# Performance work log

Hardware: AMD Instinct MI355X
Metric: run time of the kernel (lower is better)

## Reference

```python
import jax, jax.numpy as jnp
import numpy as np

N = 50000   # nodes
E = 800000  # edges (avg degree 16)
IN = 64     # in_dim
DS = 32     # in_dim // 2
HOUT = 64


def setup_inputs() -> dict:
    key = jax.random.key(0)
    ks = jax.random.split(key, 16)
    std = 0.1

    def w(k, shape):
        return std * jax.random.normal(k, shape, dtype=jnp.float32)

    z = lambda d: jnp.zeros((d,), dtype=jnp.float32)
    return {
        "x": jax.random.normal(ks[0], (N, IN), dtype=jnp.float32),
        "src": jax.random.randint(ks[1], (E,), 0, N),
        "dst": jax.random.randint(ks[2], (E,), 0, N),
        # encoders (enc_dim == in_dim branch: dim_split -> dim_split)
        "WencK": w(ks[3], (DS, DS)), "bencK": z(DS),
        "WencP1": w(ks[4], (DS, DS)), "bencP1": z(DS),
        "WencP2": w(ks[5], (DS, DS)), "bencP2": z(DS),
        # Kfun MLP: Linear(DS,HOUT) Tanh Linear(HOUT,HOUT) ReLU Linear(HOUT,HOUT)
        "WK1": w(ks[6], (DS, HOUT)), "bK1": z(HOUT),
        "WK2": w(ks[7], (HOUT, HOUT)), "bK2": z(HOUT),
        "WK3": w(ks[8], (HOUT, HOUT)), "bK3": z(HOUT),
        # Ufun MLP (same structure)
        "WU1": w(ks[9], (DS, HOUT)), "bU1": z(HOUT),
        "WU2": w(ks[10], (HOUT, HOUT)), "bU2": z(HOUT),
        "WU3": w(ks[11], (HOUT, HOUT)), "bU3": z(HOUT),
        # output heads
        "WH": w(ks[12], (HOUT, IN)), "bH": z(IN),
        "WD": w(ks[13], (IN, IN)), "bD": z(IN),
    }


def _mlp3(h, W1, b1, W2, b2, W3, b3):
    h = jnp.tanh(h @ W1 + b1)
    h = jax.nn.relu(h @ W2 + b2)
    return h @ W3 + b3


def reference(x, src, dst,
              WencK, bencK, WencP1, bencP1, WencP2, bencP2,
              WK1, bK1, WK2, bK2, WK3, bK3,
              WU1, bU1, WU2, bU2, WU3, bU3,
              WH, bH, WD, bD):
    ds = DS
    q, p = x[:, :ds], x[:, ds:]

    # getK: encode p, scatter-sum over incoming edges, node MLP
    hK = p @ WencK + bencK                              # [N, DS]
    hK_agg = jax.ops.segment_sum(hK[src], dst, num_segments=N)
    E_node = _mlp3(hK_agg, WK1, bK1, WK2, bK2, WK3, bK3)  # [N, HOUT]

    # getU: u_add_v on encoded q, edge MLP
    h1 = q @ WencP1 + bencP1
    h2 = q @ WencP2 + bencP2
    e_out = h1[src] + h2[dst]                           # [E, DS]
    E_edge = _mlp3(e_out, WU1, bU1, WU2, bU2, WU3, bU3)  # [E, HOUT]

    # getH: u_mul_e then sum into destination nodes
    E_new = jax.ops.segment_sum(E_node[src] * E_edge, dst, num_segments=N)

    # dHdx
    dH = E_new @ WH + bH                                # [N, IN]

    # get_D: dissipation term on second half of D(x), scattered over graph
    Dx = x @ WD + bD
    d_agg = jax.ops.segment_sum(Dx[:, ds:][src], dst, num_segments=N)
    d = jnp.concatenate([jnp.zeros_like(d_agg), d_agg], axis=-1)

    # dH @ J^T with J = [[0, I], [-I, 0]]  ->  [dH_p, -dH_q]
    out = jnp.concatenate([dH[:, ds:], -dH[:, :ds]], axis=-1) - d
    return out
```

## Files before the change

kernel.cpp:

```cpp
#include <hip/hip_runtime.h>
#include <hip/hip_bf16.h>

#define NN 50000
#define EE 800000
#define IN_DIM 64
#define DS_DIM 32
#define HOUT_DIM 64

#define K4_WAVES 10000
#define K4_EPW   80
#define K4_C     5

#define XA_EPW 64

#define SCAT_BLOCKS 3125
#define ENC_BLOCKS  6250

#define SCAN_NB 196

typedef __attribute__((ext_vector_type(8))) short bf16x8;
typedef __attribute__((ext_vector_type(4))) float f32x4;

__device__ __forceinline__ float fast_tanh(float x) {
    float e = __builtin_amdgcn_exp2f(x * 2.885390082f);
    return 1.f - 2.f * __builtin_amdgcn_rcpf(e + 1.f);
}

__device__ __forceinline__ void atomAddF(float* p, float v) {
#if defined(__AMDGCN__)
    unsafeAtomicAdd(p, v);
#else
    atomicAdd(p, v);
#endif
}

__device__ __forceinline__ short f2b(float f) {
    union { __hip_bfloat16 h; short s; } u;
    u.h = __float2bfloat16(f);
    return u.s;
}
__device__ __forceinline__ float b2f(unsigned short u) {
    return __uint_as_float(((unsigned int)u) << 16);
}
__device__ __forceinline__ unsigned int pack2(float lo, float hi) {
    return (unsigned int)(unsigned short)f2b(lo) | (((unsigned int)(unsigned short)f2b(hi)) << 16);
}

__global__ void khist(const int* __restrict__ dst, int* __restrict__ cnt) {
    int e = blockIdx.x * blockDim.x + threadIdx.x;
    if (e < EE) atomicAdd(&cnt[dst[e]], 1);
}

__global__ void kscanA(const int* __restrict__ cnt, int* __restrict__ blocksum) {
    __shared__ int s[256];
    int t = threadIdx.x;
    int i = blockIdx.x * 256 + t;
    s[t] = (i < NN) ? cnt[i] : 0;
    __syncthreads();
    #pragma unroll
    for (int off = 128; off > 0; off >>= 1) {
        if (t < off) s[t] += s[t + off];
        __syncthreads();
    }
    if (t == 0) blocksum[blockIdx.x] = s[0];
}

__global__ void kscanB(const int* __restrict__ blocksum, int* __restrict__ blockoff) {
    __shared__ int part[256];
    int t = threadIdx.x;
    int v = (t < SCAN_NB) ? blocksum[t] : 0;
    part[t] = v;
    __syncthreads();
    for (int off = 1; off < 256; off <<= 1) {
        int u = (t >= off) ? part[t - off] : 0;
        __syncthreads();
        part[t] += u;
        __syncthreads();
    }
    if (t < SCAN_NB) blockoff[t] = part[t] - v;
}

__global__ void kscanC(const int* __restrict__ cnt, const int* __restrict__ blockoff,
                       int* __restrict__ rowptr) {
    __shared__ int part[256];
    int t = threadIdx.x;
    int i = blockIdx.x * 256 + t;
    int v = (i < NN) ? cnt[i] : 0;
    part[t] = v;
    __syncthreads();
    for (int off = 1; off < 256; off <<= 1) {
        int u = (t >= off) ? part[t - off] : 0;
        __syncthreads();
        part[t] += u;
        __syncthreads();
    }
    if (i < NN) {
        int incl = blockoff[blockIdx.x] + part[t];
        rowptr[i] = incl - v;
        if (i == NN - 1) rowptr[NN] = incl;
    }
}

__global__ void kmega1(const int* __restrict__ src, const int* __restrict__ dst,
                       const int* __restrict__ rowptr, int* __restrict__ fill,
                       int2* __restrict__ epack,
                       const float* __restrict__ x,
                       const float* __restrict__ WencP1, const float* __restrict__ bencP1,
                       const float* __restrict__ WencP2, const float* __restrict__ bencP2,
                       __hip_bfloat16* __restrict__ h1b, __hip_bfloat16* __restrict__ h2b,
                       __hip_bfloat16* __restrict__ xb) {
    if (blockIdx.x < SCAT_BLOCKS) {
        int e = blockIdx.x * 256 + threadIdx.x;
        int d = dst[e];
        int pos = rowptr[d] + atomicAdd(&fill[d], 1);
        int2 p; p.x = src[e]; p.y = d;
        epack[pos] = p;
    } else {
        int tid = (blockIdx.x - SCAT_BLOCKS) * 256 + threadIdx.x;
        int n = tid >> 5;
        int j = tid & 31;
        if (n >= NN) return;
        const float* xr = x + (size_t)n * IN_DIM;
        float a1 = bencP1[j], a2 = bencP2[j];
        #pragma unroll
        for (int k = 0; k < 32; k++) {
            float q = xr[k];
            a1 = fmaf(q, WencP1[k * 32 + j], a1);
            a2 = fmaf(q, WencP2[k * 32 + j], a2);
        }
        union { __hip_bfloat16 h; short s; } u1, u2, u3, u4;
        u1.s = f2b(a1); u2.s = f2b(a2);
        h1b[(size_t)n * 32 + j] = u1.h;
        h2b[(size_t)n * 32 + j] = u2.h;
        u3.s = f2b(xr[j]); u4.s = f2b(xr[32 + j]);
        xb[(size_t)n * 64 + j] = u3.h;
        xb[(size_t)n * 64 + 32 + j] = u4.h;
    }
}

__global__ void __launch_bounds__(256) kxagg3(const int2* __restrict__ epack,
                                              const __hip_bfloat16* __restrict__ xb,
                                              float* __restrict__ xagg) {
    int w = (blockIdx.x * blockDim.x + threadIdx.x) >> 6;
    int lane = threadIdx.x & 63;
    int base = w * XA_EPW;
    const unsigned short* xu = reinterpret_cast<const unsigned short*>(xb);

    int2 myep = epack[base + lane];
    int sarr = myep.x, darr = myep.y;

    float v0 = b2f(xu[(size_t)__shfl(sarr, 0) * 64 + lane]);
    float v1 = b2f(xu[(size_t)__shfl(sarr, 1) * 64 + lane]);
    float v2 = b2f(xu[(size_t)__shfl(sarr, 2) * 64 + lane]);
    float v3 = b2f(xu[(size_t)__shfl(sarr, 3) * 64 + lane]);
    int cd = __shfl(darr, 0);
    float carry = 0.f;

#define XA_STEP(vv, T)                                                        \
    {                                                                         \
        float cur = vv;                                                       \
        if ((T) + 4 < XA_EPW)                                                 \
            vv = b2f(xu[(size_t)__shfl(sarr, (T) + 4) * 64 + lane]);          \
        int d = __shfl(darr, (T));                                            \
        if (d != cd) {                                                        \
            atomAddF(&xagg[(size_t)cd * 64 + lane], carry);                   \
            cd = d; carry = 0.f;                                              \
        }                                                                     \
        carry += cur;                                                         \
    }

    for (int tb = 0; tb < XA_EPW; tb += 4) {
        XA_STEP(v0, tb);
        XA_STEP(v1, tb + 1);
        XA_STEP(v2, tb + 2);
        XA_STEP(v3, tb + 3);
    }
#undef XA_STEP
    atomAddF(&xagg[(size_t)cd * 64 + lane], carry);
}

__global__ void __launch_bounds__(256) k3ab(
    const float* __restrict__ xagg, const int* __restrict__ cnt,
    const float* __restrict__ WencK, const float* __restrict__ bencK,
    const float* __restrict__ WD, const float* __restrict__ bD,
    const float* __restrict__ WK1, const float* __restrict__ bK1,
    const float* __restrict__ WK2, const float* __restrict__ bK2,
    const float* __restrict__ WK3, const float* __restrict__ bK3,
    float* __restrict__ dagg, __hip_bfloat16* __restrict__ EnodeB)
{
    __shared__ float xpose[4][16 * 68];
    const int wid  = threadIdx.x >> 6;
    const int lane = threadIdx.x & 63;
    const int g = lane >> 4;
    const int r = lane & 15;
    float* xp = xpose[wid];

    bf16x8 bwd[2][2];
    #pragma unroll
    for (int c = 0; c < 2; c++)
        #pragma unroll
        for (int nd = 0; nd < 2; nd++)
            #pragma unroll
            for (int i = 0; i < 8; i++)
                bwd[c][nd][i] = f2b(WD[(c * 32 + g * 8 + i) * 64 + 32 + nd * 16 + r]);
    bf16x8 bwk[2];
    #pragma unroll
    for (int nd = 0; nd < 2; nd++)
        #pragma unroll
        for (int i = 0; i < 8; i++)
            bwk[nd][i] = f2b(WencK[(g * 8 + i) * 32 + nd * 16 + r]);
    bf16x8 b1[4];
    #pragma unroll
    for (int nt = 0; nt < 4; nt++)
        #pragma unroll
        for (int i = 0; i < 8; i++)
            b1[nt][i] = f2b(WK1[(g * 8 + i) * 64 + nt * 16 + r]);
    bf16x8 b2[2][4], b3[2][4];
    #pragma unroll
    for (int c = 0; c < 2; c++)
        #pragma unroll
        for (int nt = 0; nt < 4; nt++)
            #pragma unroll
            for (int i = 0; i < 8; i++) {
                b2[c][nt][i] = f2b(WK2[(c * 32 + g * 8 + i) * 64 + nt * 16 + r]);
                b3[c][nt][i] = f2b(WK3[(c * 32 + g * 8 + i) * 64 + nt * 16 + r]);
            }
    float bdv[2], bkv[2];
    #pragma unroll
    for (int nd = 0; nd < 2; nd++) {
        bdv[nd] = bD[32 + nd * 16 + r];
        bkv[nd] = bencK[nd * 16 + r];
    }
    float bias1[4], bias2[4], bias3[4];
    #pragma unroll
    for (int nt = 0; nt < 4; nt++) {
        bias1[nt] = bK1[nt * 16 + r];
        bias2[nt] = bK2[nt * 16 + r];
        bias3[nt] = bK3[nt * 16 + r];
    }

    const int ntiles = NN / 16;
    const int wave = blockIdx.x * 4 + wid;
    const int nw = gridDim.x * 4;
    const f32x4 zero = {0.f, 0.f, 0.f, 0.f};

    for (int tile = wave; tile < ntiles; tile += nw) {
        bf16x8 ax0, ax1;
        {
            const float* xr = xagg + ((size_t)tile * 16 + r) * 64 + g * 8;
            float4 p0 = *reinterpret_cast<const float4*>(xr);
            float4 p1 = *reinterpret_cast<const float4*>(xr + 4);
            float4 p2 = *reinterpret_cast<const float4*>(xr + 32);
            float4 p3 = *reinterpret_cast<const float4*>(xr + 36);
            ax0[0] = f2b(p0.x); ax0[1] = f2b(p0.y); ax0[2] = f2b(p0.z); ax0[3] = f2b(p0.w);
            ax0[4] = f2b(p1.x); ax0[5] = f2b(p1.y); ax0[6] = f2b(p1.z); ax0[7] = f2b(p1.w);
            ax1[0] = f2b(p2.x); ax1[1] = f2b(p2.y); ax1[2] = f2b(p2.z); ax1[3] = f2b(p2.w);
            ax1[4] = f2b(p3.x); ax1[5] = f2b(p3.y); ax1[6] = f2b(p3.z); ax1[7] = f2b(p3.w);
        }
        float cq[4];
        #pragma unroll
        for (int q = 0; q < 4; q++) cq[q] = (float)cnt[tile * 16 + g * 4 + q];

        f32x4 accd[2];
        #pragma unroll
        for (int nd = 0; nd < 2; nd++) {
            accd[nd] = __builtin_amdgcn_mfma_f32_16x16x32_bf16(ax0, bwd[0][nd], zero, 0, 0, 0);
            accd[nd] = __builtin_amdgcn_mfma_f32_16x16x32_bf16(ax1, bwd[1][nd], accd[nd], 0, 0, 0);
        }
        #pragma unroll
        for (int nd = 0; nd < 2; nd++)
            #pragma unroll
            for (int q = 0; q < 4; q++)
                dagg[((size_t)tile * 16 + g * 4 + q) * 32 + nd * 16 + r] =
                    accd[nd][q] + cq[q] * bdv[nd];

        f32x4 acch[2];
        #pragma unroll
        for (int nd = 0; nd < 2; nd++)
            acch[nd] = __builtin_amdgcn_mfma_f32_16x16x32_bf16(ax1, bwk[nd], zero, 0, 0, 0);
        #pragma unroll
        for (int nd = 0; nd < 2; nd++)
            #pragma unroll
            for (int q = 0; q < 4; q++)
                xp[(g * 4 + q) * 68 + nd * 16 + r] = acch[nd][q] + cq[q] * bkv[nd];

        bf16x8 af;
        #pragma unroll
        for (int i = 0; i < 8; i++) af[i] = f2b(xp[r * 68 + g * 8 + i]);
        f32x4 acc[4];
        #pragma unroll
        for (int nt = 0; nt < 4; nt++)
            acc[nt] = __builtin_amdgcn_mfma_f32_16x16x32_bf16(af, b1[nt], zero, 0, 0, 0);
        #pragma unroll
        for (int nt = 0; nt < 4; nt++)
            #pragma unroll
            for (int q = 0; q < 4; q++)
                xp[(g * 4 + q) * 68 + nt * 16 + r] = fast_tanh(acc[nt][q] + bias1[nt]);

        f32x4 acc2[4] = {zero, zero, zero, zero};
        #pragma unroll
        for (int c = 0; c < 2; c++) {
            const float* row = xp + r * 68 + c * 32 + g * 8;
            bf16x8 a2;
            #pragma unroll
            for (int i = 0; i < 8; i++) a2[i] = f2b(row[i]);
            #pragma unroll
            for (int nt = 0; nt < 4; nt++)
                acc2[nt] = __builtin_amdgcn_mfma_f32_16x16x32_bf16(a2, b2[c][nt], acc2[nt], 0, 0, 0);
        }
        #pragma unroll
        for (int nt = 0; nt < 4; nt++)
            #pragma unroll
            for (int q = 0; q < 4; q++)
                xp[(g * 4 + q) * 68 + nt * 16 + r] = fmaxf(acc2[nt][q] + bias2[nt], 0.f);

        f32x4 acc3[4] = {zero, zero, zero, zero};
        #pragma unroll
        for (int c = 0; c < 2; c++) {
            const float* row = xp + r * 68 + c * 32 + g * 8;
            bf16x8 a3;
            #pragma unroll
            for (int i = 0; i < 8; i++) a3[i] = f2b(row[i]);
            #pragma unroll
            for (int nt = 0; nt < 4; nt++)
                acc3[nt] = __builtin_amdgcn_mfma_f32_16x16x32_bf16(a3, b3[c][nt], acc3[nt], 0, 0, 0);
        }
        #pragma unroll
        for (int nt = 0; nt < 4; nt++)
            #pragma unroll
            for (int q = 0; q < 4; q++)
                xp[(g * 4 + q) * 68 + nt * 16 + r] = acc3[nt][q] + bias3[nt];
        {
            const float* row = xp + r * 68 + g * 16;
            unsigned int u[8];
            #pragma unroll
            for (int i = 0; i < 8; i++) u[i] = pack2(row[2 * i], row[2 * i + 1]);
            unsigned int* ob = reinterpret_cast<unsigned int*>(EnodeB + ((size_t)tile * 16 + r) * 64 + g * 16);
            uint4 w0 = {u[0], u[1], u[2], u[3]};
            uint4 w1 = {u[4], u[5], u[6], u[7]};
            *reinterpret_cast<uint4*>(ob) = w0;
            *reinterpret_cast<uint4*>(ob + 4) = w1;
        }
    }
}

__global__ void __launch_bounds__(256) k4_mfma(
    const int2* __restrict__ epack,
    const __hip_bfloat16* __restrict__ h1b, const __hip_bfloat16* __restrict__ h2b,
    const __hip_bfloat16* __restrict__ EnodeB, float* __restrict__ Enew,
    const float* __restrict__ WU1, const float* __restrict__ bU1,
    const float* __restrict__ WU2, const float* __restrict__ bU2,
    const float* __restrict__ WU3, const float* __restrict__ bU3)
{
    __shared__ float xpose[4][16 * 68];
    const int wid  = threadIdx.x >> 6;
    const int lane = threadIdx.x & 63;
    const int g = lane >> 4;
    const int r = lane & 15;
    float* xp = xpose[wid];

    bf16x8 b1[4];
    #pragma unroll
    for (int nt = 0; nt < 4; nt++) {
        #pragma unroll
        for (int i = 0; i < 8; i++)
            b1[nt][i] = f2b(WU1[(g * 8 + i) * 64 + nt * 16 + r]);
    }
    bf16x8 b2[2][4], b3[2][4];
    #pragma unroll
    for (int c = 0; c < 2; c++) {
        #pragma unroll
        for (int nt = 0; nt < 4; nt++) {
            #pragma unroll
            for (int i = 0; i < 8; i++) {
                b2[c][nt][i] = f2b(WU2[(c * 32 + g * 8 + i) * 64 + nt * 16 + r]);
                b3[c][nt][i] = f2b(WU3[(c * 32 + g * 8 + i) * 64 + nt * 16 + r]);
            }
        }
    }
    float bias1[4], bias2[4], bias3[4];
    #pragma unroll
    for (int nt = 0; nt < 4; nt++) {
        bias1[nt] = bU1[nt * 16 + r];
        bias2[nt] = bU2[nt * 16 + r];
        bias3[nt] = bU3[nt * 16 + r];
    }

    const int wave = blockIdx.x * 4 + wid;
    const int base = wave * K4_EPW;
    const f32x4 zero = {0.f, 0.f, 0.f, 0.f};
    const unsigned short* enB = reinterpret_cast<const unsigned short*>(EnodeB);

    int   cd[4] = {-1, -1, -1, -1};
    float cv0[4] = {0, 0, 0, 0}, cv1[4] = {0, 0, 0, 0},
          cv2[4] = {0, 0, 0, 0}, cv3[4] = {0, 0, 0, 0};

    int2 ep = epack[base + r * K4_C];
    uint4 v1 = *reinterpret_cast<const uint4*>(h1b + (size_t)ep.x * 32 + g * 8);
    uint4 v2 = *reinterpret_cast<const uint4*>(h2b + (size_t)ep.y * 32 + g * 8);

    for (int t = 0; t < K4_C; t++) {
        const int s_me = ep.x, d_me = ep.y;
        union { uint4 v; unsigned int u[4]; } u1, u2;
        u1.v = v1; u2.v = v2;
        if (t + 1 < K4_C) {
            ep = epack[base + r * K4_C + t + 1];
            v1 = *reinterpret_cast<const uint4*>(h1b + (size_t)ep.x * 32 + g * 8);
            v2 = *reinterpret_cast<const uint4*>(h2b + (size_t)ep.y * 32 + g * 8);
        }

        int dq[4];
        float en0[4], en1[4], en2[4], en3[4];
        #pragma unroll
        for (int q = 0; q < 4; q++) {
            const int er = g * 4 + q;
            const int ssv = __shfl(s_me, er);
            dq[q] = __shfl(d_me, er);
            const unsigned short* enp = enB + (size_t)ssv * 64 + r;
            en0[q] = b2f(enp[0]);
            en1[q] = b2f(enp[16]);
            en2[q] = b2f(enp[32]);
            en3[q] = b2f(enp[48]);
        }

        bf16x8 a;
        #pragma unroll
        for (int w = 0; w < 4; w++) {
            float lo = b2f((unsigned short)(u1.u[w] & 0xffff)) + b2f((unsigned short)(u2.u[w] & 0xffff));
            float hi = b2f((unsigned short)(u1.u[w] >> 16))    + b2f((unsigned short)(u2.u[w] >> 16));
            a[2 * w]     = f2b(lo);
            a[2 * w + 1] = f2b(hi);
        }
        __builtin_amdgcn_s_setprio(1);
        f32x4 acc[4];
        #pragma unroll
        for (int nt = 0; nt < 4; nt++)
            acc[nt] = __builtin_amdgcn_mfma_f32_16x16x32_bf16(a, b1[nt], zero, 0, 0, 0);

        #pragma unroll
        for (int nt = 0; nt < 4; nt++) {
            #pragma unroll
            for (int q = 0; q < 4; q++)
                xp[(g * 4 + q) * 68 + nt * 16 + r] = fast_tanh(acc[nt][q] + bias1[nt]);
        }

        f32x4 acc2[4] = {zero, zero, zero, zero};
        #pragma unroll
        for (int c = 0; c < 2; c++) {
            const float* row = xp + r * 68 + c * 32 + g * 8;
            bf16x8 af;
            #pragma unroll
            for (int i = 0; i < 8; i++) af[i] = f2b(row[i]);
            #pragma unroll
            for (int nt = 0; nt < 4; nt++)
                acc2[nt] = __builtin_amdgcn_mfma_f32_16x16x32_bf16(af, b2[c][nt], acc2[nt], 0, 0, 0);
        }
        #pragma unroll
        for (int nt = 0; nt < 4; nt++) {
            #pragma unroll
            for (int q = 0; q < 4; q++)
                xp[(g * 4 + q) * 68 + nt * 16 + r] = fmaxf(acc2[nt][q] + bias2[nt], 0.f);
        }

        f32x4 acc3[4] = {zero, zero, zero, zero};
        #pragma unroll
        for (int c = 0; c < 2; c++) {
            const float* row = xp + r * 68 + c * 32 + g * 8;
            bf16x8 af;
            #pragma unroll
            for (int i = 0; i < 8; i++) af[i] = f2b(row[i]);
            #pragma unroll
            for (int nt = 0; nt < 4; nt++)
                acc3[nt] = __builtin_amdgcn_mfma_f32_16x16x32_bf16(af, b3[c][nt], acc3[nt], 0, 0, 0);
        }
        __builtin_amdgcn_s_setprio(0);

        #pragma unroll
        for (int q = 0; q < 4; q++) {
            float w0 = (acc3[0][q] + bias3[0]) * en0[q];
            float w1 = (acc3[1][q] + bias3[1]) * en1[q];
            float w2 = (acc3[2][q] + bias3[2]) * en2[q];
            float w3 = (acc3[3][q] + bias3[3]) * en3[q];
            if (dq[q] == cd[q]) {
                cv0[q] += w0; cv1[q] += w1; cv2[q] += w2; cv3[q] += w3;
            } else {
                if (cd[q] >= 0) {
                    float* ew = Enew + (size_t)cd[q] * 64 + r;
                    atomAddF(ew,      cv0[q]);
                    atomAddF(ew + 16, cv1[q]);
                    atomAddF(ew + 32, cv2[q]);
                    atomAddF(ew + 48, cv3[q]);
                }
                cd[q] = dq[q];
                cv0[q] = w0; cv1[q] = w1; cv2[q] = w2; cv3[q] = w3;
            }
        }
    }
    #pragma unroll
    for (int q = 0; q < 4; q++) {
        if (cd[q] >= 0) {
            float* ew = Enew + (size_t)cd[q] * 64 + r;
            atomAddF(ew,      cv0[q]);
            atomAddF(ew + 16, cv1[q]);
            atomAddF(ew + 32, cv2[q]);
            atomAddF(ew + 48, cv3[q]);
        }
    }
}

__global__ void k5_out(const float* __restrict__ Enew, const float* __restrict__ dagg,
                       const float* __restrict__ WH, const float* __restrict__ bH,
                       float* __restrict__ out) {
    int tid = blockIdx.x * blockDim.x + threadIdx.x;
    int n = tid >> 6;
    int j = tid & 63;
    if (n >= NN) return;
    const float* er = Enew + (size_t)n * 64;
    int jj = (j < 32) ? (j + 32) : (j - 32);
    float acc = bH[jj];
    #pragma unroll
    for (int k = 0; k < 64; k++) acc = fmaf(er[k], WH[k * 64 + jj], acc);
    float val;
    if (j < 32) val = acc;
    else        val = -acc - dagg[(size_t)n * 32 + (j - 32)];
    out[tid] = val;
}

extern "C" void kernel_launch(void* const* d_in, const int* in_sizes, int n_in,
                              void* d_out, int out_size, void* d_ws, size_t ws_size,
                              hipStream_t stream) {
    const float* x      = (const float*)d_in[0];
    const int*   src    = (const int*)d_in[1];
    const int*   dst    = (const int*)d_in[2];
    const float* WencK  = (const float*)d_in[3];
    const float* bencK  = (const float*)d_in[4];
    const float* WencP1 = (const float*)d_in[5];
    const float* bencP1 = (const float*)d_in[6];
    const float* WencP2 = (const float*)d_in[7];
    const float* bencP2 = (const float*)d_in[8];
    const float* WK1    = (const float*)d_in[9];
    const float* bK1    = (const float*)d_in[10];
    const float* WK2    = (const float*)d_in[11];
    const float* bK2    = (const float*)d_in[12];
    const float* WK3    = (const float*)d_in[13];
    const float* bK3    = (const float*)d_in[14];
    const float* WU1    = (const float*)d_in[15];
    const float* bU1    = (const float*)d_in[16];
    const float* WU2    = (const float*)d_in[17];
    const float* bU2    = (const float*)d_in[18];
    const float* WU3    = (const float*)d_in[19];
    const float* bU3    = (const float*)d_in[20];
    const float* WH     = (const float*)d_in[21];
    const float* bH     = (const float*)d_in[22];
    const float* WD     = (const float*)d_in[23];
    const float* bD     = (const float*)d_in[24];
    float* out = (float*)d_out;

    float* buf0 = (float*)d_ws;
    float* dagg = buf0 + (size_t)NN * 64;
    __hip_bfloat16* h1b    = (__hip_bfloat16*)(dagg + (size_t)NN * 32);
    __hip_bfloat16* h2b    = h1b + (size_t)NN * 32;
    __hip_bfloat16* EnodeB = h2b + (size_t)NN * 32;
    __hip_bfloat16* xb     = EnodeB + (size_t)NN * 64;
    int*  cnt      = (int*)(xb + (size_t)NN * 64);
    int*  fill     = cnt + NN;
    int*  rowptr   = fill + NN;
    int*  blocksum = rowptr + NN + 2;
    int*  blockoff = blocksum + 256;
    int2* epack    = (int2*)(blockoff + 256);
    size_t need = (size_t)NN * 96 * 4 + (size_t)NN * 192 * 2
                + ((size_t)NN * 3 + 2 + 512) * 4 + (size_t)EE * 8;
    if (ws_size < need) return;

    hipMemsetAsync(cnt, 0, (size_t)2 * NN * sizeof(int), stream);
    hipMemsetAsync(buf0, 0, (size_t)NN * 64 * sizeof(float), stream);

    khist<<<(EE + 255) / 256, 256, 0, stream>>>(dst, cnt);
    kscanA<<<SCAN_NB, 256, 0, stream>>>(cnt, blocksum);
    kscanB<<<1, 256, 0, stream>>>(blocksum, blockoff);
    kscanC<<<SCAN_NB, 256, 0, stream>>>(cnt, blockoff, rowptr);
    kmega1<<<SCAT_BLOCKS + ENC_BLOCKS, 256, 0, stream>>>(
        src, dst, rowptr, fill, epack, x, WencP1, bencP1, WencP2, bencP2, h1b, h2b, xb);
    kxagg3<<<(EE / XA_EPW) / 4, 256, 0, stream>>>(epack, xb, buf0);
    k3ab<<<782, 256, 0, stream>>>(buf0, cnt, WencK, bencK, WD, bD,
                                  WK1, bK1, WK2, bK2, WK3, bK3, dagg, EnodeB);
    hipMemsetAsync(buf0, 0, (size_t)NN * 64 * sizeof(float), stream);
    k4_mfma<<<K4_WAVES / 4, 256, 0, stream>>>(epack, h1b, h2b, EnodeB, buf0,
                                              WU1, bU1, WU2, bU2, WU3, bU3);
    k5_out<<<(NN * 64 + 255) / 256, 256, 0, stream>>>(buf0, dagg, WH, bH, out);
}
```

Before: 294.9 us.

## Fuse histogram with encoder, store MLP staging as bf16, add XCD block swizzle

Moves the node-encoder work into the histogram kernel so it overlaps the atomic count pass, and leaves the edge scatter as its own small kernel. LDS transpose buffers in the MLP kernels now hold bf16 instead of fp32, so each A-fragment is one vector load rather than eight scalar loads plus conversions. Block indices in the edge-walking kernels are remapped so contiguous ranges of waves land on the same XCD, which should improve L2 locality. Separate workspaces for xagg and Enew replace the second mid-pipeline memset with one larger upfront memset.

```diff
diff --git a/kernel.cpp b/kernel.cpp
--- a/kernel.cpp
+++ b/kernel.cpp
@@ -10,13 +10,17 @@
 #define K4_WAVES 10000
 #define K4_EPW   80
 #define K4_C     5
+#define K4_NWG   (K4_WAVES / 4)
 
 #define XA_EPW 64
-
-#define SCAT_BLOCKS 3125
+#define XA_NWG 3125
+
+#define HIST_BLOCKS 3125
 #define ENC_BLOCKS  6250
 
 #define SCAN_NB 196
+
+#define XPS 72
 
 typedef __attribute__((ext_vector_type(8))) short bf16x8;
 typedef __attribute__((ext_vector_type(4))) float f32x4;
@@ -42,13 +46,43 @@
 __device__ __forceinline__ float b2f(unsigned short u) {
     return __uint_as_float(((unsigned int)u) << 16);
 }
-__device__ __forceinline__ unsigned int pack2(float lo, float hi) {
-    return (unsigned int)(unsigned short)f2b(lo) | (((unsigned int)(unsigned short)f2b(hi)) << 16);
-}
-
-__global__ void khist(const int* __restrict__ dst, int* __restrict__ cnt) {
-    int e = blockIdx.x * blockDim.x + threadIdx.x;
-    if (e < EE) atomicAdd(&cnt[dst[e]], 1);
+
+__device__ __forceinline__ int xcd_swz(int bid, int nwg) {
+    int xcd = bid & 7, idx = bid >> 3;
+    int q = nwg >> 3, r = nwg & 7;
+    return (xcd < r ? xcd * (q + 1) : r * (q + 1) + (xcd - r) * q) + idx;
+}
+
+__global__ void kmega0(const int* __restrict__ dst, int* __restrict__ cnt,
+                       const float* __restrict__ x,
+                       const float* __restrict__ WencP1, const float* __restrict__ bencP1,
+                       const float* __restrict__ WencP2, const float* __restrict__ bencP2,
+                       __hip_bfloat16* __restrict__ h1b, __hip_bfloat16* __restrict__ h2b,
+                       __hip_bfloat16* __restrict__ xb) {
+    if (blockIdx.x < HIST_BLOCKS) {
+        int e = blockIdx.x * 256 + threadIdx.x;
+        atomicAdd(&cnt[dst[e]], 1);
+    } else {
+        int tid = (blockIdx.x - HIST_BLOCKS) * 256 + threadIdx.x;
+        int n = tid >> 5;
+        int j = tid & 31;
+        if (n >= NN) return;
+        const float* xr = x + (size_t)n * IN_DIM;
+        float a1 = bencP1[j], a2 = bencP2[j];
+        #pragma unroll
+        for (int k = 0; k < 32; k++) {
+            float q = xr[k];
+            a1 = fmaf(q, WencP1[k * 32 + j], a1);
+            a2 = fmaf(q, WencP2[k * 32 + j], a2);
+        }
+        union { __hip_bfloat16 h; short s; } u1, u2, u3, u4;
+        u1.s = f2b(a1); u2.s = f2b(a2);
+        h1b[(size_t)n * 32 + j] = u1.h;
+        h2b[(size_t)n * 32 + j] = u2.h;
+        u3.s = f2b(xr[j]); u4.s = f2b(xr[32 + j]);
+        xb[(size_t)n * 64 + j] = u3.h;
+        xb[(size_t)n * 64 + 32 + j] = u4.h;
+    }
 }
 
 __global__ void kscanA(const int* __restrict__ cnt, int* __restrict__ blocksum) {
@@ -101,47 +135,22 @@
     }
 }
 
-__global__ void kmega1(const int* __restrict__ src, const int* __restrict__ dst,
-                       const int* __restrict__ rowptr, int* __restrict__ fill,
-                       int2* __restrict__ epack,
-                       const float* __restrict__ x,
-                       const float* __restrict__ WencP1, const float* __restrict__ bencP1,
-                       const float* __restrict__ WencP2, const float* __restrict__ bencP2,
-                       __hip_bfloat16* __restrict__ h1b, __hip_bfloat16* __restrict__ h2b,
-                       __hip_bfloat16* __restrict__ xb) {
-    if (blockIdx.x < SCAT_BLOCKS) {
-        int e = blockIdx.x * 256 + threadIdx.x;
-        int d = dst[e];
-        int pos = rowptr[d] + atomicAdd(&fill[d], 1);
-        int2 p; p.x = src[e]; p.y = d;
-        epack[pos] = p;
-    } else {
-        int tid = (blockIdx.x - SCAT_BLOCKS) * 256 + threadIdx.x;
-        int n = tid >> 5;
-        int j = tid & 31;
-        if (n >= NN) return;
-        const float* xr = x + (size_t)n * IN_DIM;
-        float a1 = bencP1[j], a2 = bencP2[j];
-        #pragma unroll
-        for (int k = 0; k < 32; k++) {
-            float q = xr[k];
-            a1 = fmaf(q, WencP1[k * 32 + j], a1);
-            a2 = fmaf(q, WencP2[k * 32 + j], a2);
-        }
-        union { __hip_bfloat16 h; short s; } u1, u2, u3, u4;
-        u1.s = f2b(a1); u2.s = f2b(a2);
-        h1b[(size_t)n * 32 + j] = u1.h;
-        h2b[(size_t)n * 32 + j] = u2.h;
-        u3.s = f2b(xr[j]); u4.s = f2b(xr[32 + j]);
-        xb[(size_t)n * 64 + j] = u3.h;
-        xb[(size_t)n * 64 + 32 + j] = u4.h;
-    }
+__global__ void kscatter(const int* __restrict__ src, const int* __restrict__ dst,
+                         const int* __restrict__ rowptr, int* __restrict__ fill,
+                         int2* __restrict__ epack) {
+    int e = blockIdx.x * 256 + threadIdx.x;
+    if (e >= EE) return;
+    int d = dst[e];
+    int pos = rowptr[d] + atomicAdd(&fill[d], 1);
+    int2 p; p.x = src[e]; p.y = d;
+    epack[pos] = p;
 }
 
 __global__ void __launch_bounds__(256) kxagg3(const int2* __restrict__ epack,
                                               const __hip_bfloat16* __restrict__ xb,
                                               float* __restrict__ xagg) {
-    int w = (blockIdx.x * blockDim.x + threadIdx.x) >> 6;
+    int sbid = xcd_swz(blockIdx.x, XA_NWG);
+    int w = sbid * 4 + (threadIdx.x >> 6);
     int lane = threadIdx.x & 63;
     int base = w * XA_EPW;
     const unsigned short* xu = reinterpret_cast<const unsigned short*>(xb);
@@ -188,12 +197,12 @@
     const float* __restrict__ WK3, const float* __restrict__ bK3,
     float* __restrict__ dagg, __hip_bfloat16* __restrict__ EnodeB)
 {
-    __shared__ float xpose[4][16 * 68];
+    __shared__ unsigned short xpose[4][16 * XPS];
     const int wid  = threadIdx.x >> 6;
     const int lane = threadIdx.x & 63;
     const int g = lane >> 4;
     const int r = lane & 15;
-    float* xp = xpose[wid];
+    unsigned short* xp = xpose[wid];
 
     bf16x8 bwd[2][2];
     #pragma unroll
@@ -282,11 +291,9 @@
         for (int nd = 0; nd < 2; nd++)
             #pragma unroll
             for (int q = 0; q < 4; q++)
-                xp[(g * 4 + q) * 68 + nd * 16 + r] = acch[nd][q] + cq[q] * bkv[nd];
-
-        bf16x8 af;
-        #pragma unroll
-        for (int i = 0; i < 8; i++) af[i] = f2b(xp[r * 68 + g * 8 + i]);
+                xp[(g * 4 + q) * XPS + nd * 16 + r] = (unsigned short)f2b(acch[nd][q] + cq[q] * bkv[nd]);
+
+        bf16x8 af = *reinterpret_cast<const bf16x8*>(xp + r * XPS + g * 8);
         f32x4 acc[4];
         #pragma unroll
         for (int nt = 0; nt < 4; nt++)
@@ -295,15 +302,12 @@
         for (int nt = 0; nt < 4; nt++)
             #pragma unroll
             for (int q = 0; q < 4; q++)
-                xp[(g * 4 + q) * 68 + nt * 16 + r] = fast_tanh(acc[nt][q] + bias1[nt]);
+                xp[(g * 4 + q) * XPS + nt * 16 + r] = (unsigned short)f2b(fast_tanh(acc[nt][q] + bias1[nt]));
 
         f32x4 acc2[4] = {zero, zero, zero, zero};
         #pragma unroll
         for (int c = 0; c < 2; c++) {
-            const float* row = xp + r * 68 + c * 32 + g * 8;
-            bf16x8 a2;
-            #pragma unroll
-            for (int i = 0; i < 8; i++) a2[i] = f2b(row[i]);
+            bf16x8 a2 = *reinterpret_cast<const bf16x8*>(xp + r * XPS + c * 32 + g * 8);
             #pragma unroll
             for (int nt = 0; nt < 4; nt++)
                 acc2[nt] = __builtin_amdgcn_mfma_f32_16x16x32_bf16(a2, b2[c][nt], acc2[nt], 0, 0, 0);
@@ -312,15 +316,12 @@
         for (int nt = 0; nt < 4; nt++)
             #pragma unroll
             for (int q = 0; q < 4; q++)
-                xp[(g * 4 + q) * 68 + nt * 16 + r] = fmaxf(acc2[nt][q] + bias2[nt], 0.f);
+                xp[(g * 4 + q) * XPS + nt * 16 + r] = (unsigned short)f2b(fmaxf(acc2[nt][q] + bias2[nt], 0.f));
 
         f32x4 acc3[4] = {zero, zero, zero, zero};
         #pragma unroll
         for (int c = 0; c < 2; c++) {
-            const float* row = xp + r * 68 + c * 32 + g * 8;
-            bf16x8 a3;
-            #pragma unroll
-            for (int i = 0; i < 8; i++) a3[i] = f2b(row[i]);
+            bf16x8 a3 = *reinterpret_cast<const bf16x8*>(xp + r * XPS + c * 32 + g * 8);
             #pragma unroll
             for (int nt = 0; nt < 4; nt++)
                 acc3[nt] = __builtin_amdgcn_mfma_f32_16x16x32_bf16(a3, b3[c][nt], acc3[nt], 0, 0, 0);
@@ -329,15 +330,11 @@
         for (int nt = 0; nt < 4; nt++)
             #pragma unroll
             for (int q = 0; q < 4; q++)
-                xp[(g * 4 + q) * 68 + nt * 16 + r] = acc3[nt][q] + bias3[nt];
+                xp[(g * 4 + q) * XPS + nt * 16 + r] = (unsigned short)f2b(acc3[nt][q] + bias3[nt]);
         {
-            const float* row = xp + r * 68 + g * 16;
-            unsigned int u[8];
-            #pragma unroll
-            for (int i = 0; i < 8; i++) u[i] = pack2(row[2 * i], row[2 * i + 1]);
+            uint4 w0 = *reinterpret_cast<const uint4*>(xp + r * XPS + g * 16);
+            uint4 w1 = *reinterpret_cast<const uint4*>(xp + r * XPS + g * 16 + 8);
             unsigned int* ob = reinterpret_cast<unsigned int*>(EnodeB + ((size_t)tile * 16 + r) * 64 + g * 16);
-            uint4 w0 = {u[0], u[1], u[2], u[3]};
-            uint4 w1 = {u[4], u[5], u[6], u[7]};
             *reinterpret_cast<uint4*>(ob) = w0;
             *reinterpret_cast<uint4*>(ob + 4) = w1;
         }
@@ -352,12 +349,12 @@
     const float* __restrict__ WU2, const float* __restrict__ bU2,
     const float* __restrict__ WU3, const float* __restrict__ bU3)
 {
-    __shared__ float xpose[4][16 * 68];
+    __shared__ unsigned short xpose[4][16 * XPS];
     const int wid  = threadIdx.x >> 6;
     const int lane = threadIdx.x & 63;
     const int g = lane >> 4;
     const int r = lane & 15;
-    float* xp = xpose[wid];
+    unsigned short* xp = xpose[wid];
 
     bf16x8 b1[4];
     #pragma unroll
@@ -386,7 +383,8 @@
         bias3[nt] = bU3[nt * 16 + r];
     }
 
-    const int wave = blockIdx.x * 4 + wid;
+    const int sbid = xcd_swz(blockIdx.x, K4_NWG);
+    const int wave = sbid * 4 + wid;
     const int base = wave * K4_EPW;
     const f32x4 zero = {0.f, 0.f, 0.f, 0.f};
     const unsigned short* enB = reinterpret_cast<const unsigned short*>(EnodeB);
@@ -441,16 +439,13 @@
         for (int nt = 0; nt < 4; nt++) {
             #pragma unroll
             for (int q = 0; q < 4; q++)
-                xp[(g * 4 + q) * 68 + nt * 16 + r] = fast_tanh(acc[nt][q] + bias1[nt]);
+                xp[(g * 4 + q) * XPS + nt * 16 + r] = (unsigned short)f2b(fast_tanh(acc[nt][q] + bias1[nt]));
         }
 
         f32x4 acc2[4] = {zero, zero, zero, zero};
         #pragma unroll
         for (int c = 0; c < 2; c++) {
-            const float* row = xp + r * 68 + c * 32 + g * 8;
-            bf16x8 af;
-            #pragma unroll
-            for (int i = 0; i < 8; i++) af[i] = f2b(row[i]);
+            bf16x8 af = *reinterpret_cast<const bf16x8*>(xp + r * XPS + c * 32 + g * 8);
             #pragma unroll
             for (int nt = 0; nt < 4; nt++)
                 acc2[nt] = __builtin_amdgcn_mfma_f32_16x16x32_bf16(af, b2[c][nt], acc2[nt], 0, 0, 0);
@@ -459,16 +454,13 @@
         for (int nt = 0; nt < 4; nt++) {
             #pragma unroll
             for (int q = 0; q < 4; q++)
-                xp[(g * 4 + q) * 68 + nt * 16 + r] = fmaxf(acc2[nt][q] + bias2[nt], 0.f);
+                xp[(g * 4 + q) * XPS + nt * 16 + r] = (unsigned short)f2b(fmaxf(acc2[nt][q] + bias2[nt], 0.f));
         }
 
         f32x4 acc3[4] = {zero, zero, zero, zero};
         #pragma unroll
         for (int c = 0; c < 2; c++) {
-            const float* row = xp + r * 68 + c * 32 + g * 8;
-            bf16x8 af;
-            #pragma unroll
-            for (int i = 0; i < 8; i++) af[i] = f2b(row[i]);
+            bf16x8 af = *reinterpret_cast<const bf16x8*>(xp + r * XPS + c * 32 + g * 8);
             #pragma unroll
             for (int nt = 0; nt < 4; nt++)
                 acc3[nt] = __builtin_amdgcn_mfma_f32_16x16x32_bf16(af, b3[c][nt], acc3[nt], 0, 0, 0);
@@ -556,8 +548,9 @@
     const float* bD     = (const float*)d_in[24];
     float* out = (float*)d_out;
 
-    float* buf0 = (float*)d_ws;
-    float* dagg = buf0 + (size_t)NN * 64;
+    float* xagg = (float*)d_ws;
+    float* Enew = xagg + (size_t)NN * 64;
+    float* dagg = Enew + (size_t)NN * 64;
     __hip_bfloat16* h1b    = (__hip_bfloat16*)(dagg + (size_t)NN * 32);
     __hip_bfloat16* h2b    = h1b + (size_t)NN * 32;
     __hip_bfloat16* EnodeB = h2b + (size_t)NN * 32;
@@ -568,24 +561,23 @@
     int*  blocksum = rowptr + NN + 2;
     int*  blockoff = blocksum + 256;
     int2* epack    = (int2*)(blockoff + 256);
-    size_t need = (size_t)NN * 96 * 4 + (size_t)NN * 192 * 2
+    size_t need = (size_t)NN * 160 * 4 + (size_t)NN * 192 * 2
                 + ((size_t)NN * 3 + 2 + 512) * 4 + (size_t)EE * 8;
     if (ws_size < need) return;
 
     hipMemsetAsync(cnt, 0, (size_t)2 * NN * sizeof(int), stream);
-    hipMemsetAsync(buf0, 0, (size_t)NN * 64 * sizeof(float), stream);
-
-    khist<<<(EE + 255) / 256, 256, 0, stream>>>(dst, cnt);
+    hipMemsetAsync(xagg, 0, (size_t)NN * 128 * sizeof(float), stream);
+
+    kmega0<<<HIST_BLOCKS + ENC_BLOCKS, 256, 0, stream>>>(
+        dst, cnt, x, WencP1, bencP1, WencP2, bencP2, h1b, h2b, xb);
     kscanA<<<SCAN_NB, 256, 0, stream>>>(cnt, blocksum);
     kscanB<<<1, 256, 0, stream>>>(blocksum, blockoff);
     kscanC<<<SCAN_NB, 256, 0, stream>>>(cnt, blockoff, rowptr);
-    kmega1<<<SCAT_BLOCKS + ENC_BLOCKS, 256, 0, stream>>>(
-        src, dst, rowptr, fill, epack, x, WencP1, bencP1, WencP2, bencP2, h1b, h2b, xb);
-    kxagg3<<<(EE / XA_EPW) / 4, 256, 0, stream>>>(epack, xb, buf0);
-    k3ab<<<782, 256, 0, stream>>>(buf0, cnt, WencK, bencK, WD, bD,
+    kscatter<<<HIST_BLOCKS, 256, 0, stream>>>(src, dst, rowptr, fill, epack);
+    kxagg3<<<XA_NWG, 256, 0, stream>>>(epack, xb, xagg);
+    k3ab<<<782, 256, 0, stream>>>(xagg, cnt, WencK, bencK, WD, bD,
                                   WK1, bK1, WK2, bK2, WK3, bK3, dagg, EnodeB);
-    hipMemsetAsync(buf0, 0, (size_t)NN * 64 * sizeof(float), stream);
-    k4_mfma<<<K4_WAVES / 4, 256, 0, stream>>>(epack, h1b, h2b, EnodeB, buf0,
-                                              WU1, bU1, WU2, bU2, WU3, bU3);
-    k5_out<<<(NN * 64 + 255) / 256, 256, 0, stream>>>(buf0, dagg, WH, bH, out);
-}
+    k4_mfma<<<K4_NWG, 256, 0, stream>>>(epack, h1b, h2b, EnodeB, Enew,
+                                        WU1, bU1, WU2, bU2, WU3, bU3);
+    k5_out<<<(NN * 64 + 255) / 256, 256, 0, stream>>>(Enew, dagg, WH, bH, out);
+}
```

Measured after the change: 289.4 us. No clear change (-1.9%).
